# Kernel optimization log

Hardware: AMD Instinct MI355X
Metric: run time of the kernel (lower is better)

## Reference

```python
import jax, jax.numpy as jnp
import numpy as np

NEG = 9999.0
EPS = 1e-8  # torch CosineSimilarity default eps


def _attend_head(x, v, W_out, b_out):
    # x: [B, n, D]; row 0 is the node, rows 1: are neighbours
    node = x[:, 0, :]            # [B, D]
    neigh = x[:, 1:, :]          # [B, n-1, D]
    scores = jnp.einsum('bnd,bd->bn', neigh, node)  # [B, n-1]
    # masked_softmax: positions with exactly-zero score get -9999 added
    masked = scores + (jnp.where(scores != 0, 0.0, -1.0) * NEG)
    aw = jax.nn.softmax(masked, axis=-1)            # [B, n-1]
    context = jnp.einsum('n,bn,bnd->bd', v, aw, neigh)  # [B, D]
    feat = jnp.concatenate([node, context], axis=1)     # [B, 2D]
    return feat @ W_out.T + b_out                       # [B, 300]


def _cosine(a, b):
    na = jnp.maximum(jnp.linalg.norm(a, axis=1), EPS)
    nb = jnp.maximum(jnp.linalg.norm(b, axis=1), EPS)
    return jnp.sum(a * b, axis=1) / (na * nb)


def setup_inputs() -> dict:
    key = jax.random.key(0)
    ks = jax.random.split(key, 8)
    B, n, V, D = 4096, 32, 100000, 512
    inputs = jax.random.randint(ks[0], (B, 2, n), 0, V, dtype=jnp.int64)
    inputs_prop = jax.random.randint(ks[1], (B, 2, 3, n), 0, V, dtype=jnp.int64)
    emb = jax.random.normal(ks[2], (V, D), dtype=jnp.float32)
    W_out = jax.random.normal(ks[3], (300, 2 * D), dtype=jnp.float32) * 0.02
    b_out = jax.random.normal(ks[4], (300,), dtype=jnp.float32) * 0.02
    v = jnp.full((n - 1,), 1.0 / (n - 1), dtype=jnp.float32)
    W_prop = jax.random.normal(ks[5], (300, 600 + D), dtype=jnp.float32) * 0.02
    b_prop = jax.random.normal(ks[6], (300,), dtype=jnp.float32) * 0.02
    return {"inputs": inputs, "inputs_prop": inputs_prop, "emb": emb,
            "W_out": W_out, "b_out": b_out, "v": v,
            "W_prop": W_prop, "b_prop": b_prop}


def reference(inputs, inputs_prop, emb, W_out, b_out, v, W_prop, b_prop):
    # entity branch
    results = []
    for i in range(2):
        x = emb[inputs[:, i, :]]                 # [B, n, D]
        results.append(_attend_head(x, v, W_out, b_out))
    # property branch
    prop_vecs = []
    for i in range(2):
        xp = emb[inputs_prop[:, i]]              # [B, 3, n, D]
        dom = _attend_head(xp[:, 1], v, W_out, b_out)   # domain
        rng = _attend_head(xp[:, 2], v, W_out, b_out)   # range
        prp = xp[:, 0, 0, :]                     # property embedding [B, D]
        feat = jnp.concatenate([dom, rng, prp], axis=1)  # [B, 1112]
        prop_vecs.append(feat @ W_prop.T + b_prop)
    x_ent = _cosine(results[0], results[1])
    x_prop = _cosine(prop_vecs[0], prop_vecs[1])
    return jnp.concatenate([x_ent, x_prop])
```

## Files before the change

### kernel.cpp

```cpp
#include <hip/hip_runtime.h>

typedef _Float16 f16x8 __attribute__((ext_vector_type(8)));
typedef _Float16 f16x4 __attribute__((ext_vector_type(4)));
typedef float    f32x4 __attribute__((ext_vector_type(4)));

#define EMBH_OFF  0ULL
#define CTXH_OFF  102400000ULL
#define APH_OFF   127565824ULL
#define WH_OFF    138051584ULL
#define WPH_OFF   138706944ULL
#define HEAD_OFF  139444224ULL
#define PROP_OFF  149274624ULL
#define NIDX_OFF  159105024ULL
#define PIDX_OFF  159203328ULL

__device__ __forceinline__ void gload16h(const _Float16* g, _Float16* l) {
    __builtin_amdgcn_global_load_lds(
        (const __attribute__((address_space(1))) unsigned int*)g,
        (__attribute__((address_space(3))) unsigned int*)l, 16, 0, 0);
}

__global__ __launch_bounds__(256) void conv_kernel(
    const float* __restrict__ emb, const float* __restrict__ W_out,
    const float* __restrict__ W_prop,
    _Float16* __restrict__ embh, _Float16* __restrict__ Wh, _Float16* __restrict__ Wph)
{
    const int N_EMB4 = 12800000;
    const int N_WH4  = 81920;
    const int N_WPH4 = 92160;
    int stride = gridDim.x * 256;
    for (int id = blockIdx.x * 256 + threadIdx.x; id < N_EMB4 + N_WH4 + N_WPH4; id += stride) {
        float4 f; _Float16* dst;
        if (id < N_EMB4) {
            f = ((const float4*)emb)[id];
            dst = embh + (size_t)id * 4;
        } else if (id < N_EMB4 + N_WH4) {
            int id2 = id - N_EMB4;
            int n = id2 >> 8, c4 = id2 & 255;
            f = (n < 300) ? ((const float4*)W_out)[n * 256 + c4] : make_float4(0.f,0.f,0.f,0.f);
            dst = Wh + (size_t)id2 * 4;
        } else {
            int id3 = id - N_EMB4 - N_WH4;
            int n = id3 / 288, c4 = id3 - n * 288;
            if (n >= 300 || (c4 >= 150 && c4 < 160)) f = make_float4(0.f,0.f,0.f,0.f);
            else if (c4 < 150) f = ((const float4*)W_prop)[n * 278 + c4];
            else               f = ((const float4*)W_prop)[n * 278 + c4 - 10];
            dst = Wph + (size_t)id3 * 4;
        }
        f16x4 h = { (_Float16)f.x, (_Float16)f.y, (_Float16)f.z, (_Float16)f.w };
        *(f16x4*)dst = h;
    }
}

__global__ __launch_bounds__(256) void attend_kernel(
    const int* __restrict__ inputs,
    const int* __restrict__ inputs_prop,
    const _Float16* __restrict__ embh,
    const float* __restrict__ v,
    _Float16* __restrict__ ctxh,
    int* __restrict__ nidx, int* __restrict__ pidx,
    _Float16* __restrict__ Aph)
{
    int w    = blockIdx.x * 4 + (threadIdx.x >> 6);
    int lane = threadIdx.x & 63;
    int h = w >> 12;
    int b = w & 4095;

    int base, i = 0;
    const int* ip;
    if (h < 2) { base = (b * 2 + h) * 32; ip = inputs; }
    else {
        i = (h - 2) >> 1;
        int s = 1 + ((h - 2) & 1);
        base = ((b * 2 + i) * 3 + s) * 32;
        ip = inputs_prop;
    }

    int myidx = 0;
    if (lane < 32) myidx = ip[base + lane];
    int idx0 = __shfl(myidx, 0);
    if (lane == 0) {
        nidx[w] = idx0;
        if (h == 2 || h == 4) pidx[i * 4096 + b] = inputs_prop[((b * 2 + i) * 3) * 32];
    }

    const f16x8* e8 = (const f16x8*)embh;
    f16x8 n8 = e8[(size_t)idx0 * 64 + lane];
    float nf[8];
    #pragma unroll
    for (int q = 0; q < 8; ++q) nf[q] = (float)n8[q];

    f16x8 pe[4];
    #pragma unroll
    for (int j = 1; j <= 4; ++j) {
        int ij = __shfl(myidx, j);
        pe[(j - 1) & 3] = e8[(size_t)ij * 64 + lane];
    }

    float m = -3.0e38f, den = 0.0f;
    float c[8] = {0.f,0.f,0.f,0.f,0.f,0.f,0.f,0.f};

    #pragma unroll
    for (int j = 1; j < 32; ++j) {
        const int slot = (j - 1) & 3;
        f16x8 ev = pe[slot];
        if (j + 4 < 32) {
            int ijn = __shfl(myidx, j + 4);
            pe[slot] = e8[(size_t)ijn * 64 + lane];
        }
        float ef[8];
        #pragma unroll
        for (int q = 0; q < 8; ++q) ef[q] = (float)ev[q];
        float p = ef[0]*nf[0] + ef[1]*nf[1] + ef[2]*nf[2] + ef[3]*nf[3]
                + ef[4]*nf[4] + ef[5]*nf[5] + ef[6]*nf[6] + ef[7]*nf[7];
        #pragma unroll
        for (int d = 1; d < 64; d <<= 1) p += __shfl_xor(p, d);

        float s = (p != 0.0f) ? p : -9999.0f;
        if (s - m > 8.0f) {
            float scale = __expf(m - s);
            den *= scale;
            #pragma unroll
            for (int q = 0; q < 8; ++q) c[q] *= scale;
            m = s;
        }
        float e = __expf(s - m);
        den += e;
        float we = v[j - 1] * e;
        #pragma unroll
        for (int q = 0; q < 8; ++q) c[q] += we * ef[q];
    }
    float inv = 1.0f / den;
    f16x8 co;
    #pragma unroll
    for (int q = 0; q < 8; ++q) co[q] = (_Float16)(c[q] * inv);
    __builtin_nontemporal_store(co, (f16x8*)(ctxh + (size_t)w * 512 + lane * 8));

    if ((h == 2 || h == 4) && lane < 5) {
        f16x8 z = {};
        __builtin_nontemporal_store(z, (f16x8*)(Aph + (size_t)(i * 4096 + b) * 640 + 600 + lane * 8));
    }
}

__global__ __launch_bounds__(256) void gemm_head_kernel(
    const _Float16* __restrict__ embh, const _Float16* __restrict__ ctxh,
    const int* __restrict__ nidx, const _Float16* __restrict__ Wh,
    const float* __restrict__ bias, float* __restrict__ outf,
    _Float16* __restrict__ Aph)
{
    __shared__ _Float16 Ash[128 * 64], Bsh[64 * 64];
    __shared__ int sN[128];

    int t = threadIdx.x, lane = t & 63, wid = t >> 6;
    int wm = wid >> 1, wn = wid & 1;
    int m0 = blockIdx.y * 128, n0 = blockIdx.x * 64;
    if (t < 128) sN[t] = nidx[m0 + t];
    __syncthreads();

    f32x4 acc[4][2];
    #pragma unroll
    for (int mf = 0; mf < 4; ++mf)
        #pragma unroll
        for (int nf = 0; nf < 2; ++nf) acc[mf][nf] = (f32x4){0.f,0.f,0.f,0.f};

    int rowq = lane >> 3, cq = lane & 7;
    int cqs = cq ^ rowq;

    for (int k0 = 0; k0 < 1024; k0 += 64) {
        #pragma unroll
        for (int qq = 0; qq < 6; ++qq) {
            int q = wid * 6 + qq;
            if (q < 16) {
                int row = q * 8 + rowq;
                if (k0 < 512) gload16h(embh + (size_t)sN[row] * 512 + k0 + cqs * 8, Ash + q * 512);
                else          gload16h(ctxh + (size_t)(m0 + row) * 512 + (k0 - 512) + cqs * 8, Ash + q * 512);
            } else {
                int j = q - 16, row = j * 8 + rowq;
                gload16h(Wh + (size_t)(n0 + row) * 1024 + k0 + cqs * 8, Bsh + j * 512);
            }
        }
        __syncthreads();

        int l15 = lane & 15, hi = lane >> 4, l7 = lane & 7;
        #pragma unroll
        for (int s = 0; s < 2; ++s) {
            int sw = ((s * 4 + hi) ^ l7) * 8;
            f16x8 a[4], bb[2];
            #pragma unroll
            for (int mf = 0; mf < 4; ++mf)
                a[mf] = *(const f16x8*)&Ash[((wm * 4 + mf) * 16 + l15) * 64 + sw];
            #pragma unroll
            for (int nf = 0; nf < 2; ++nf)
                bb[nf] = *(const f16x8*)&Bsh[((wn * 2 + nf) * 16 + l15) * 64 + sw];
            #pragma unroll
            for (int mf = 0; mf < 4; ++mf)
                #pragma unroll
                for (int nf = 0; nf < 2; ++nf)
                    acc[mf][nf] = __builtin_amdgcn_mfma_f32_16x16x32_f16(a[mf], bb[nf], acc[mf][nf], 0, 0, 0);
        }
        __syncthreads();
    }

    #pragma unroll
    for (int mf = 0; mf < 4; ++mf)
        #pragma unroll
        for (int nf = 0; nf < 2; ++nf) {
            int n = n0 + wn * 32 + nf * 16 + (lane & 15);
            if (n >= 300) continue;
            int rowbase = m0 + (wm * 4 + mf) * 16 + ((lane >> 4) << 2);
            float bv = bias[n];
            #pragma unroll
            for (int r = 0; r < 4; ++r) {
                float val = acc[mf][nf][r] + bv;
                int mm = rowbase + r;
                int h = mm >> 12;
                if (h < 2) {
                    outf[(size_t)mm * 300 + n] = val;
                } else {
                    int i = (h - 2) >> 1;
                    int col = ((h - 2) & 1) ? 300 + n : n;
                    Aph[(size_t)(i * 4096 + (mm & 4095)) * 640 + col] = (_Float16)val;
                }
            }
        }
}

__global__ __launch_bounds__(256) void gemm_prop_kernel(
    const _Float16* __restrict__ Aph, const int* __restrict__ pidx,
    const _Float16* __restrict__ embh, const _Float16* __restrict__ Wph,
    const float* __restrict__ bias, float* __restrict__ outf)
{
    __shared__ _Float16 Ash[64 * 64], Bsh[64 * 64];
    __shared__ int sPid[64];

    int t = threadIdx.x, lane = t & 63, wid = t >> 6;
    int wm = wid >> 1, wn = wid & 1;
    int m0 = blockIdx.y * 64, n0 = blockIdx.x * 64;
    if (t < 64) {
        int mm = m0 + t;
        sPid[t] = pidx[(mm >> 12) * 4096 + (mm & 4095)];
    }
    __syncthreads();

    f32x4 acc[2][2];
    #pragma unroll
    for (int mf = 0; mf < 2; ++mf)
        #pragma unroll
        for (int nf = 0; nf < 2; ++nf) acc[mf][nf] = (f32x4){0.f,0.f,0.f,0.f};

    int rowq = lane >> 3, cq = lane & 7;
    int cqs = cq ^ rowq;

    for (int k0 = 0; k0 < 1152; k0 += 64) {
        #pragma unroll
        for (int qq = 0; qq < 4; ++qq) {
            int q = wid * 4 + qq;
            if (q < 8) {
                int row = q * 8 + rowq;
                if (k0 < 640) gload16h(Aph + (size_t)(m0 + row) * 640 + k0 + cqs * 8, Ash + q * 512);
                else          gload16h(embh + (size_t)sPid[row] * 512 + (k0 - 640) + cqs * 8, Ash + q * 512);
            } else {
                int j = q - 8, row = j * 8 + rowq;
                gload16h(Wph + (size_t)(n0 + row) * 1152 + k0 + cqs * 8, Bsh + j * 512);
            }
        }
        __syncthreads();

        int l15 = lane & 15, hi = lane >> 4, l7 = lane & 7;
        #pragma unroll
        for (int s = 0; s < 2; ++s) {
            int sw = ((s * 4 + hi) ^ l7) * 8;
            f16x8 a[2], bb[2];
            #pragma unroll
            for (int mf = 0; mf < 2; ++mf)
                a[mf] = *(const f16x8*)&Ash[((wm * 2 + mf) * 16 + l15) * 64 + sw];
            #pragma unroll
            for (int nf = 0; nf < 2; ++nf)
                bb[nf] = *(const f16x8*)&Bsh[((wn * 2 + nf) * 16 + l15) * 64 + sw];
            #pragma unroll
            for (int mf = 0; mf < 2; ++mf)
                #pragma unroll
                for (int nf = 0; nf < 2; ++nf)
                    acc[mf][nf] = __builtin_amdgcn_mfma_f32_16x16x32_f16(a[mf], bb[nf], acc[mf][nf], 0, 0, 0);
        }
        __syncthreads();
    }

    #pragma unroll
    for (int mf = 0; mf < 2; ++mf)
        #pragma unroll
        for (int nf = 0; nf < 2; ++nf) {
            int n = n0 + wn * 32 + nf * 16 + (lane & 15);
            if (n >= 300) continue;
            int rowbase = m0 + (wm * 2 + mf) * 16 + ((lane >> 4) << 2);
            float bv = bias[n];
            #pragma unroll
            for (int r = 0; r < 4; ++r)
                outf[(size_t)(rowbase + r) * 300 + n] = acc[mf][nf][r] + bv;
        }
}

__global__ __launch_bounds__(256) void cosine_kernel(
    const float* __restrict__ head_out,
    const float* __restrict__ prop_out,
    float* __restrict__ out)
{
    int w    = blockIdx.x * 4 + (threadIdx.x >> 6);
    int lane = threadIdx.x & 63;
    const float *a, *b;
    if (w < 4096) {
        a = head_out + (size_t)w * 300;
        b = head_out + (size_t)(4096 + w) * 300;
    } else {
        int b2 = w - 4096;
        a = prop_out + (size_t)b2 * 300;
        b = prop_out + (size_t)(4096 + b2) * 300;
    }
    float ab = 0.f, aa = 0.f, bb = 0.f;
    for (int tt = lane; tt < 300; tt += 64) {
        float av = a[tt], bv = b[tt];
        ab += av * bv; aa += av * av; bb += bv * bv;
    }
    #pragma unroll
    for (int d = 1; d < 64; d <<= 1) {
        ab += __shfl_xor(ab, d);
        aa += __shfl_xor(aa, d);
        bb += __shfl_xor(bb, d);
    }
    if (lane == 0) {
        float na = fmaxf(sqrtf(aa), 1e-8f);
        float nb = fmaxf(sqrtf(bb), 1e-8f);
        out[w] = ab / (na * nb);
    }
}

extern "C" void kernel_launch(void* const* d_in, const int* in_sizes, int n_in,
                              void* d_out, int out_size, void* d_ws, size_t ws_size,
                              hipStream_t stream) {
    const int*   inputs      = (const int*)d_in[0];
    const int*   inputs_prop = (const int*)d_in[1];
    const float* emb         = (const float*)d_in[2];
    const float* W_out       = (const float*)d_in[3];
    const float* b_out       = (const float*)d_in[4];
    const float* v           = (const float*)d_in[5];
    const float* W_prop      = (const float*)d_in[6];
    const float* b_prop      = (const float*)d_in[7];
    float* out = (float*)d_out;

    char* ws = (char*)d_ws;
    _Float16* embh = (_Float16*)(ws + EMBH_OFF);
    _Float16* ctxh = (_Float16*)(ws + CTXH_OFF);
    _Float16* Aph  = (_Float16*)(ws + APH_OFF);
    _Float16* Wh   = (_Float16*)(ws + WH_OFF);
    _Float16* Wph  = (_Float16*)(ws + WPH_OFF);
    float* head_out = (float*)(ws + HEAD_OFF);
    float* prop_out = (float*)(ws + PROP_OFF);
    int*   nidx     = (int*)(ws + NIDX_OFF);
    int*   pidx     = (int*)(ws + PIDX_OFF);

    conv_kernel<<<8192, 256, 0, stream>>>(emb, W_out, W_prop, embh, Wh, Wph);
    attend_kernel<<<6144, 256, 0, stream>>>(inputs, inputs_prop, embh, v, ctxh, nidx, pidx, Aph);
    gemm_head_kernel<<<dim3(5, 192), 256, 0, stream>>>(embh, ctxh, nidx, Wh, b_out, head_out, Aph);
    gemm_prop_kernel<<<dim3(5, 128), 256, 0, stream>>>(Aph, pidx, embh, Wph, b_prop, prop_out);
    cosine_kernel<<<2048, 256, 0, stream>>>(head_out, prop_out, out);
}
```

Baseline: 240.8 us.

## Give each GEMM block the full output width and use fdot2 in attention

Both output GEMMs are retiled so each block covers all 300 (padded to 320) output columns for a smaller row tile. The gathered embedding and context rows of A are then loaded once per row rather than once per 64-column tile, at the cost of a larger LDS footprint for the B tile and fewer, heavier blocks. Separately, the attention dot product uses packed fp16 dot2 instructions instead of converting each element to fp32 before multiplying. The dot2 path changes the rounding order of the scores slightly.

```diff
diff --git a/kernel.cpp b/kernel.cpp
--- a/kernel.cpp
+++ b/kernel.cpp
@@ -2,6 +2,7 @@
 
 typedef _Float16 f16x8 __attribute__((ext_vector_type(8)));
 typedef _Float16 f16x4 __attribute__((ext_vector_type(4)));
+typedef _Float16 f16x2 __attribute__((ext_vector_type(2)));
 typedef float    f32x4 __attribute__((ext_vector_type(4)));
 
 #define EMBH_OFF  0ULL
@@ -86,9 +87,6 @@
 
     const f16x8* e8 = (const f16x8*)embh;
     f16x8 n8 = e8[(size_t)idx0 * 64 + lane];
-    float nf[8];
-    #pragma unroll
-    for (int q = 0; q < 8; ++q) nf[q] = (float)n8[q];
 
     f16x8 pe[4];
     #pragma unroll
@@ -108,11 +106,16 @@
             int ijn = __shfl(myidx, j + 4);
             pe[slot] = e8[(size_t)ijn * 64 + lane];
         }
-        float ef[8];
-        #pragma unroll
-        for (int q = 0; q < 8; ++q) ef[q] = (float)ev[q];
-        float p = ef[0]*nf[0] + ef[1]*nf[1] + ef[2]*nf[2] + ef[3]*nf[3]
-                + ef[4]*nf[4] + ef[5]*nf[5] + ef[6]*nf[6] + ef[7]*nf[7];
+        float p = 0.0f;
+        const f16x2* na = (const f16x2*)&n8;
+        const f16x2* ea = (const f16x2*)&ev;
+#if __has_builtin(__builtin_amdgcn_fdot2)
+        #pragma unroll
+        for (int q = 0; q < 4; ++q) p = __builtin_amdgcn_fdot2(ea[q], na[q], p, false);
+#else
+        #pragma unroll
+        for (int q = 0; q < 8; ++q) p += (float)ev[q] * (float)n8[q];
+#endif
         #pragma unroll
         for (int d = 1; d < 64; d <<= 1) p += __shfl_xor(p, d);
 
@@ -128,7 +131,7 @@
         den += e;
         float we = v[j - 1] * e;
         #pragma unroll
-        for (int q = 0; q < 8; ++q) c[q] += we * ef[q];
+        for (int q = 0; q < 8; ++q) c[q] += we * (float)ev[q];
     }
     float inv = 1.0f / den;
     f16x8 co;
@@ -148,81 +151,72 @@
     const float* __restrict__ bias, float* __restrict__ outf,
     _Float16* __restrict__ Aph)
 {
-    __shared__ _Float16 Ash[128 * 64], Bsh[64 * 64];
-    __shared__ int sN[128];
+    __shared__ _Float16 Ash[64 * 64];
+    __shared__ _Float16 Bsh[320 * 64];
+    __shared__ int sN[64];
 
     int t = threadIdx.x, lane = t & 63, wid = t >> 6;
-    int wm = wid >> 1, wn = wid & 1;
-    int m0 = blockIdx.y * 128, n0 = blockIdx.x * 64;
-    if (t < 128) sN[t] = nidx[m0 + t];
+    int m0 = blockIdx.x * 64;
+    if (t < 64) sN[t] = nidx[m0 + t];
     __syncthreads();
 
-    f32x4 acc[4][2];
-    #pragma unroll
-    for (int mf = 0; mf < 4; ++mf)
-        #pragma unroll
-        for (int nf = 0; nf < 2; ++nf) acc[mf][nf] = (f32x4){0.f,0.f,0.f,0.f};
+    f32x4 acc[20];
+    #pragma unroll
+    for (int nf = 0; nf < 20; ++nf) acc[nf] = (f32x4){0.f,0.f,0.f,0.f};
 
     int rowq = lane >> 3, cq = lane & 7;
     int cqs = cq ^ rowq;
+    int l15 = lane & 15, hi = lane >> 4, l7 = lane & 7;
 
     for (int k0 = 0; k0 < 1024; k0 += 64) {
         #pragma unroll
-        for (int qq = 0; qq < 6; ++qq) {
-            int q = wid * 6 + qq;
-            if (q < 16) {
+        for (int qq = 0; qq < 12; ++qq) {
+            int q = wid * 12 + qq;
+            if (q < 8) {
                 int row = q * 8 + rowq;
                 if (k0 < 512) gload16h(embh + (size_t)sN[row] * 512 + k0 + cqs * 8, Ash + q * 512);
                 else          gload16h(ctxh + (size_t)(m0 + row) * 512 + (k0 - 512) + cqs * 8, Ash + q * 512);
             } else {
-                int j = q - 16, row = j * 8 + rowq;
-                gload16h(Wh + (size_t)(n0 + row) * 1024 + k0 + cqs * 8, Bsh + j * 512);
+                int j = q - 8;
+                int row = j * 8 + rowq;
+                gload16h(Wh + (size_t)row * 1024 + k0 + cqs * 8, Bsh + j * 512);
             }
         }
         __syncthreads();
 
-        int l15 = lane & 15, hi = lane >> 4, l7 = lane & 7;
         #pragma unroll
         for (int s = 0; s < 2; ++s) {
             int sw = ((s * 4 + hi) ^ l7) * 8;
-            f16x8 a[4], bb[2];
+            f16x8 a = *(const f16x8*)&Ash[(wid * 16 + l15) * 64 + sw];
             #pragma unroll
-            for (int mf = 0; mf < 4; ++mf)
-                a[mf] = *(const f16x8*)&Ash[((wm * 4 + mf) * 16 + l15) * 64 + sw];
-            #pragma unroll
-            for (int nf = 0; nf < 2; ++nf)
-                bb[nf] = *(const f16x8*)&Bsh[((wn * 2 + nf) * 16 + l15) * 64 + sw];
-            #pragma unroll
-            for (int mf = 0; mf < 4; ++mf)
-                #pragma unroll
-                for (int nf = 0; nf < 2; ++nf)
-                    acc[mf][nf] = __builtin_amdgcn_mfma_f32_16x16x32_f16(a[mf], bb[nf], acc[mf][nf], 0, 0, 0);
+            for (int nf = 0; nf < 20; ++nf) {
+                f16x8 bb = *(const f16x8*)&Bsh[(nf * 16 + l15) * 64 + sw];
+                acc[nf] = __builtin_amdgcn_mfma_f32_16x16x32_f16(a, bb, acc[nf], 0, 0, 0);
+            }
         }
         __syncthreads();
     }
 
-    #pragma unroll
-    for (int mf = 0; mf < 4; ++mf)
-        #pragma unroll
-        for (int nf = 0; nf < 2; ++nf) {
-            int n = n0 + wn * 32 + nf * 16 + (lane & 15);
-            if (n >= 300) continue;
-            int rowbase = m0 + (wm * 4 + mf) * 16 + ((lane >> 4) << 2);
-            float bv = bias[n];
-            #pragma unroll
-            for (int r = 0; r < 4; ++r) {
-                float val = acc[mf][nf][r] + bv;
-                int mm = rowbase + r;
-                int h = mm >> 12;
-                if (h < 2) {
-                    outf[(size_t)mm * 300 + n] = val;
-                } else {
-                    int i = (h - 2) >> 1;
-                    int col = ((h - 2) & 1) ? 300 + n : n;
-                    Aph[(size_t)(i * 4096 + (mm & 4095)) * 640 + col] = (_Float16)val;
-                }
-            }
-        }
+    int h = (m0 >> 12);
+    #pragma unroll
+    for (int nf = 0; nf < 20; ++nf) {
+        int n = nf * 16 + l15;
+        if (n >= 300) continue;
+        int rowbase = m0 + wid * 16 + (hi << 2);
+        float bv = bias[n];
+        #pragma unroll
+        for (int r = 0; r < 4; ++r) {
+            float val = acc[nf][r] + bv;
+            int mm = rowbase + r;
+            if (h < 2) {
+                outf[(size_t)mm * 300 + n] = val;
+            } else {
+                int i = (h - 2) >> 1;
+                int col = ((h - 2) & 1) ? 300 + n : n;
+                Aph[(size_t)(i * 4096 + (mm & 4095)) * 640 + col] = (_Float16)val;
+            }
+        }
+    }
 }
 
 __global__ __launch_bounds__(256) void gemm_prop_kernel(
@@ -230,74 +224,66 @@
     const _Float16* __restrict__ embh, const _Float16* __restrict__ Wph,
     const float* __restrict__ bias, float* __restrict__ outf)
 {
-    __shared__ _Float16 Ash[64 * 64], Bsh[64 * 64];
-    __shared__ int sPid[64];
+    __shared__ _Float16 Ash[32 * 64];
+    __shared__ _Float16 Bsh[320 * 64];
+    __shared__ int sPid[32];
 
     int t = threadIdx.x, lane = t & 63, wid = t >> 6;
     int wm = wid >> 1, wn = wid & 1;
-    int m0 = blockIdx.y * 64, n0 = blockIdx.x * 64;
-    if (t < 64) {
+    int m0 = blockIdx.x * 32;
+    if (t < 32) {
         int mm = m0 + t;
         sPid[t] = pidx[(mm >> 12) * 4096 + (mm & 4095)];
     }
     __syncthreads();
 
-    f32x4 acc[2][2];
-    #pragma unroll
-    for (int mf = 0; mf < 2; ++mf)
-        #pragma unroll
-        for (int nf = 0; nf < 2; ++nf) acc[mf][nf] = (f32x4){0.f,0.f,0.f,0.f};
+    f32x4 acc[10];
+    #pragma unroll
+    for (int nf = 0; nf < 10; ++nf) acc[nf] = (f32x4){0.f,0.f,0.f,0.f};
 
     int rowq = lane >> 3, cq = lane & 7;
     int cqs = cq ^ rowq;
+    int l15 = lane & 15, hi = lane >> 4, l7 = lane & 7;
 
     for (int k0 = 0; k0 < 1152; k0 += 64) {
         #pragma unroll
-        for (int qq = 0; qq < 4; ++qq) {
-            int q = wid * 4 + qq;
-            if (q < 8) {
+        for (int qq = 0; qq < 11; ++qq) {
+            int q = wid * 11 + qq;
+            if (q < 4) {
                 int row = q * 8 + rowq;
                 if (k0 < 640) gload16h(Aph + (size_t)(m0 + row) * 640 + k0 + cqs * 8, Ash + q * 512);
                 else          gload16h(embh + (size_t)sPid[row] * 512 + (k0 - 640) + cqs * 8, Ash + q * 512);
-            } else {
-                int j = q - 8, row = j * 8 + rowq;
-                gload16h(Wph + (size_t)(n0 + row) * 1152 + k0 + cqs * 8, Bsh + j * 512);
+            } else if (q < 44) {
+                int j = q - 4;
+                int row = j * 8 + rowq;
+                gload16h(Wph + (size_t)row * 1152 + k0 + cqs * 8, Bsh + j * 512);
             }
         }
         __syncthreads();
 
-        int l15 = lane & 15, hi = lane >> 4, l7 = lane & 7;
         #pragma unroll
         for (int s = 0; s < 2; ++s) {
             int sw = ((s * 4 + hi) ^ l7) * 8;
-            f16x8 a[2], bb[2];
+            f16x8 a = *(const f16x8*)&Ash[(wm * 16 + l15) * 64 + sw];
             #pragma unroll
-            for (int mf = 0; mf < 2; ++mf)
-                a[mf] = *(const f16x8*)&Ash[((wm * 2 + mf) * 16 + l15) * 64 + sw];
-            #pragma unroll
-            for (int nf = 0; nf < 2; ++nf)
-                bb[nf] = *(const f16x8*)&Bsh[((wn * 2 + nf) * 16 + l15) * 64 + sw];
-            #pragma unroll
-            for (int mf = 0; mf < 2; ++mf)
-                #pragma unroll
-                for (int nf = 0; nf < 2; ++nf)
-                    acc[mf][nf] = __builtin_amdgcn_mfma_f32_16x16x32_f16(a[mf], bb[nf], acc[mf][nf], 0, 0, 0);
+            for (int nf = 0; nf < 10; ++nf) {
+                f16x8 bb = *(const f16x8*)&Bsh[((wn * 10 + nf) * 16 + l15) * 64 + sw];
+                acc[nf] = __builtin_amdgcn_mfma_f32_16x16x32_f16(a, bb, acc[nf], 0, 0, 0);
+            }
         }
         __syncthreads();
     }
 
     #pragma unroll
-    for (int mf = 0; mf < 2; ++mf)
-        #pragma unroll
-        for (int nf = 0; nf < 2; ++nf) {
-            int n = n0 + wn * 32 + nf * 16 + (lane & 15);
-            if (n >= 300) continue;
-            int rowbase = m0 + (wm * 2 + mf) * 16 + ((lane >> 4) << 2);
-            float bv = bias[n];
-            #pragma unroll
-            for (int r = 0; r < 4; ++r)
-                outf[(size_t)(rowbase + r) * 300 + n] = acc[mf][nf][r] + bv;
-        }
+    for (int nf = 0; nf < 10; ++nf) {
+        int n = wn * 160 + nf * 16 + l15;
+        if (n >= 300) continue;
+        int rowbase = m0 + wm * 16 + (hi << 2);
+        float bv = bias[n];
+        #pragma unroll
+        for (int r = 0; r < 4; ++r)
+            outf[(size_t)(rowbase + r) * 300 + n] = acc[nf][r] + bv;
+    }
 }
 
 __global__ __launch_bounds__(256) void cosine_kernel(
@@ -360,7 +346,7 @@
 
     conv_kernel<<<8192, 256, 0, stream>>>(emb, W_out, W_prop, embh, Wh, Wph);
     attend_kernel<<<6144, 256, 0, stream>>>(inputs, inputs_prop, embh, v, ctxh, nidx, pidx, Aph);
-    gemm_head_kernel<<<dim3(5, 192), 256, 0, stream>>>(embh, ctxh, nidx, Wh, b_out, head_out, Aph);
-    gemm_prop_kernel<<<dim3(5, 128), 256, 0, stream>>>(Aph, pidx, embh, Wph, b_prop, prop_out);
+    gemm_head_kernel<<<384, 256, 0, stream>>>(embh, ctxh, nidx, Wh, b_out, head_out, Aph);
+    gemm_prop_kernel<<<256, 256, 0, stream>>>(Aph, pidx, embh, Wph, b_prop, prop_out);
     cosine_kernel<<<2048, 256, 0, stream>>>(head_out, prop_out, out);
 }
```

New measurement: 242.1 us. No clear change (+0.5%).
